# Optimization experiments

Measured on AMD Instinct MI355X. Metric: run time of the kernel, lower is better.

Reference implementation:

```python
import jax, jax.numpy as jnp
import numpy as np

THRESH = 0.3
OUT_THRESH = 0.3
LENS = 0.5  # surrogate-gradient window (ActFun in snn-delays repo)


@jax.custom_vjp
def spike(x):
    # Heaviside spike with rectangular surrogate gradient
    return (x > 0.0).astype(x.dtype)

def _spike_fwd(x):
    return spike(x), x

def _spike_bwd(x, g):
    return (g * (jnp.abs(x) < LENS).astype(g.dtype),)

spike.defvjp(_spike_fwd, _spike_bwd)


def setup_inputs() -> dict:
    key = jax.random.key(0)
    ks = jax.random.split(key, 7)
    B, T, I, H, O = 256, 50, 1024, 2048, 20
    # binary input spikes (rate ~0.2), as an SNN would receive
    inp = (jax.random.uniform(ks[0], (B, T, I)) < 0.2).astype(jnp.float32)
    # Linear(in, out, bias=False) -> weight [out, in], Kaiming-uniform-ish init
    w_ih = jax.random.uniform(ks[1], (H, I), minval=-1.0, maxval=1.0) / np.sqrt(I)
    w_hh = jax.random.uniform(ks[2], (H, H), minval=-1.0, maxval=1.0) / np.sqrt(H)
    w_ho = jax.random.uniform(ks[3], (O, H), minval=-1.0, maxval=1.0) / np.sqrt(H)
    tau_m_h = 0.83 + 0.1 * jax.random.normal(ks[4], (H,))
    tau_m_o = 0.83 + 0.1 * jax.random.normal(ks[5], (O,))
    return {"input": inp, "w_ih": w_ih, "w_hh": w_hh, "w_ho": w_ho,
            "tau_m_h": tau_m_h, "tau_m_o": tau_m_o}


def _rsnn_forward(inp, w_ih, w_hh, w_ho, tau_m_h, tau_m_o):
    B, T, I = inp.shape
    H = w_ih.shape[0]
    O = w_ho.shape[0]
    alpha_h = jnp.exp(-1.0 / tau_m_h)  # [H]
    alpha_o = jnp.exp(-1.0 / tau_m_o)  # [O]
    zH = jnp.zeros((B, H), inp.dtype)
    zO = jnp.zeros((B, O), inp.dtype)

    def step(carry, x_t):
        h_mem, h_spk, o_mem, o_spk, o_sum, mot = carry
        # hidden membrane update: input + recurrent + decayed (reset-gated) mem
        h_mem = (x_t @ w_ih.T) + (h_spk @ w_hh.T) + h_mem * alpha_h * (1.0 - h_spk)
        h_spk = spike(h_mem - THRESH)
        # output membrane update
        o_mem = o_mem * alpha_o * (1.0 - o_spk) + h_spk @ w_ho.T
        o_spk = spike(o_mem - OUT_THRESH)
        o_sum = o_sum + o_spk
        mot = mot + jax.nn.softmax(o_mem, axis=1)
        return (h_mem, h_spk, o_mem, o_spk, o_sum, mot), None

    init = (zH, zH, zO, zO, zO, zO)
    (h_mem, h_spk, o_mem, o_spk, o_sum, mot), _ = jax.lax.scan(
        step, init, jnp.swapaxes(inp, 0, 1))  # scan over time [T,B,I]
    return o_sum / T, mot


def reference(input, w_ih, w_hh, w_ho, tau_m_h, tau_m_o):
    return _rsnn_forward(input, w_ih, w_hh, w_ho, tau_m_h, tau_m_o)
```

## Files before the change

kernel.cpp:

```cpp
#include <hip/hip_runtime.h>
#include <stdint.h>
#include <math.h>


#define B_   256
#define T_   50
#define I_   1024
#define H_   2048
#define O_   20
#define XIN_T  262144
#define XS_BUF 524288
#define WNT 589824
#define WPL 196608

typedef __attribute__((ext_vector_type(4))) int intx4;
typedef long long ll_t;

__device__ __forceinline__ int digit_of(float v, int p) {
  int W = (int)rintf(v * 134217728.0f);
  int c0 = ((W + 128) & 255) - 128;
  int W1 = (W - c0) >> 8;
  int c1 = ((W1 + 128) & 255) - 128;
  int W2 = (W1 - c1) >> 8;
  return (p == 0) ? c0 : (p == 1) ? c1 : W2;
}

__global__ void prep_w(const float* __restrict__ w_ih,
                       const float* __restrict__ w_hh,
                       int8_t* __restrict__ Wtl) {
  int blk = blockIdx.x;
  int n = blk / 9, kg = blk % 9;
  int k9 = (kg * 256 + (int)threadIdx.x) * 4;
  int p = k9 / 3072, kk = k9 % 3072;
  const float* src = (kk < 1024) ? (w_ih + n * I_ + kk)
                                 : (w_hh + n * H_ + (kk - 1024));
  float4 v = *(const float4*)src;
  int d0 = digit_of(v.x, p) & 255;
  int d1 = digit_of(v.y, p) & 255;
  int d2 = digit_of(v.z, p) & 255;
  int d3 = digit_of(v.w, p) & 255;
  int packed = d0 | (d1 << 8) | (d2 << 16) | (d3 << 24);
  size_t off = (size_t)(n >> 6) * WNT + (size_t)p * WPL + (kk >> 6) * 4096 +
               (n & 63) * 64 + (kk & 63);
  *(int*)(Wtl + off) = packed;
}

__global__ void init_k(int8_t* __restrict__ Xin, int8_t* __restrict__ Xs,
                       float* __restrict__ Hm, const float* __restrict__ input,
                       const float* __restrict__ tau_h,
                       const float* __restrict__ tau_o,
                       float* __restrict__ AlphaH, float* __restrict__ AlphaO,
                       const float* __restrict__ w_ho, double* __restrict__ WhoD,
                       float* __restrict__ Om, float* __restrict__ Osp,
                       float* __restrict__ Osu, float* __restrict__ Mo) {
  int id = blockIdx.x * 256 + threadIdx.x;
  {
    int b = id >> 8, i4 = (id & 255) * 4;
    for (int t = 0; t < T_; ++t) {
      float4 v = *(const float4*)(input + ((size_t)(b * T_ + t) << 10) + i4);
      uchar4 pk;
      pk.x = v.x > 0.5f ? 1 : 0;
      pk.y = v.y > 0.5f ? 1 : 0;
      pk.z = v.z > 0.5f ? 1 : 0;
      pk.w = v.w > 0.5f ? 1 : 0;
      *(uchar4*)(Xin + (size_t)t * XIN_T + (b >> 6) * 65536 + (i4 >> 6) * 4096 +
                 (b & 63) * 64 + (i4 & 63)) = pk;
    }
  }
  *(double*)(Xs + (size_t)id * 8) = 0.0;
  *(float4*)(Hm + (size_t)id * 8) = make_float4(0.f, 0.f, 0.f, 0.f);
  *(float4*)(Hm + (size_t)id * 8 + 4) = make_float4(0.f, 0.f, 0.f, 0.f);
  if (id < 32 * O_ * 64) {
    int nt = id / 1280, rem = id % 1280, o = rem / 64, hl = rem & 63;
    WhoD[id] = (double)w_ho[o * H_ + nt * 64 + hl];
  }
  if (id < H_) AlphaH[id] = (float)exp((double)(-1.0f / tau_h[id]));
  if (id < O_) AlphaO[id] = (float)exp((double)(-1.0f / tau_o[id]));
  if (id < B_ * O_) {
    Om[id] = 0.f; Osp[id] = 0.f; Osu[id] = 0.f; Mo[id] = 0.f;
  }
}

__global__ __launch_bounds__(512, 1) void step_k(
    const int8_t* __restrict__ Wtl, const int8_t* __restrict__ Xin,
    int8_t* __restrict__ Xs, float* __restrict__ Hm, double* __restrict__ Po,
    const double* __restrict__ WhoD, const float* __restrict__ AlphaH,
    const float* __restrict__ AlphaO, float* __restrict__ Om,
    float* __restrict__ Osp, float* __restrict__ Osu, float* __restrict__ Mo,
    int t) {
  __shared__ double WhoL[1280];
  __shared__ __align__(16) int8_t red[49152];
  __shared__ int8_t spk_lT[2048];
  __shared__ float om_l[O_];

  const int j = blockIdx.x;
  const int nt = (j & 7) * 4 + (j >> 6);
  const int mt = (j >> 3) & 7;
  const int tid = threadIdx.x;
  const int l = tid & 63, wv = tid >> 6;
  const int c = wv >> 2, k = wv & 3;
  const int r_ = l & 15, q = l >> 4;

  for (int i = tid; i < 1280; i += 512) WhoL[i] = WhoD[nt * 1280 + i];

  if (t > 0 && tid < O_) {
    const double* pp = Po + ((size_t)(((t - 1) & 1) * 256 + j) * 32) * 20 + tid;
    double s = 0.0;
#pragma unroll
    for (int n2 = 0; n2 < 32; ++n2) s += pp[n2 * 20];
    float r = (float)s;
    float m = Om[j * O_ + tid] * AlphaO[tid] * (1.0f - Osp[j * O_ + tid]) + r;
    om_l[tid] = m;
  }
  __syncthreads();
  if (t > 0 && tid < O_) {
    float m = om_l[tid];
    float mx = om_l[0];
#pragma unroll
    for (int o = 1; o < O_; ++o) mx = fmaxf(mx, om_l[o]);
    float se = 0.f;
#pragma unroll
    for (int o = 0; o < O_; ++o) se += expf(om_l[o] - mx);
    float sp = (m - 0.3f) > 0.f ? 1.f : 0.f;
    Om[j * O_ + tid] = m;
    Osp[j * O_ + tid] = sp;
    Osu[j * O_ + tid] += sp;
    Mo[j * O_ + tid] += expf(m - mx) / se;
  }

  const int arow = ((mt & 1) * 32 + r_) * 64 + q * 16;
  const int8_t* Ain = Xin + (size_t)t * XIN_T + (mt >> 1) * 65536 + arow;
  const int8_t* Asp = Xs + (size_t)(t & 1) * XS_BUF + (mt >> 1) * 131072 + arow;
  const int8_t* Bw = Wtl + (size_t)nt * WNT + (c * 32 + r_) * 64 + q * 16;
  const int u0 = k * 12;

  intx4 acc[2][2][3];
#pragma unroll
  for (int fr = 0; fr < 2; ++fr)
#pragma unroll
    for (int fc = 0; fc < 2; ++fc)
#pragma unroll
      for (int p = 0; p < 3; ++p) acc[fr][fc][p] = (intx4){0, 0, 0, 0};

  intx4 a[2][2], b[2][2][3];
  {
    const int8_t* ap = (u0 < 16) ? (Ain + u0 * 4096) : (Asp + (u0 - 16) * 4096);
    a[0][0] = *(const intx4*)ap;
    a[0][1] = *(const intx4*)(ap + 1024);
    const int8_t* bp = Bw + u0 * 4096;
#pragma unroll
    for (int p = 0; p < 3; ++p)
#pragma unroll
      for (int fc = 0; fc < 2; ++fc)
        b[0][fc][p] = *(const intx4*)(bp + p * WPL + fc * 1024);
  }
#pragma unroll
  for (int i = 0; i < 12; ++i) {
    const int cur = i & 1, nxt = cur ^ 1;
    if (i < 11) {
      const int un = u0 + i + 1;
      const int8_t* ap = (un < 16) ? (Ain + un * 4096) : (Asp + (un - 16) * 4096);
      a[nxt][0] = *(const intx4*)ap;
      a[nxt][1] = *(const intx4*)(ap + 1024);
      const int8_t* bp = Bw + un * 4096;
#pragma unroll
      for (int p = 0; p < 3; ++p)
#pragma unroll
        for (int fc = 0; fc < 2; ++fc)
          b[nxt][fc][p] = *(const intx4*)(bp + p * WPL + fc * 1024);
    }
#pragma unroll
    for (int p = 0; p < 3; ++p)
#pragma unroll
      for (int fc = 0; fc < 2; ++fc) {
        acc[0][fc][p] = __builtin_amdgcn_mfma_i32_16x16x64_i8(
            a[cur][0], b[cur][fc][p], acc[0][fc][p], 0, 0, 0);
        acc[1][fc][p] = __builtin_amdgcn_mfma_i32_16x16x64_i8(
            a[cur][1], b[cur][fc][p], acc[1][fc][p], 0, 0, 0);
      }
  }

#define REDP(s, idx) (red + (((c * 2 + (s)) * 12 + (idx)) * 64 + l) * 16)
  if (k == 1 || k == 3) {
    const int s = k >> 1;
#pragma unroll
    for (int fr = 0; fr < 2; ++fr)
#pragma unroll
      for (int fc = 0; fc < 2; ++fc)
#pragma unroll
        for (int p = 0; p < 3; ++p)
          *(intx4*)REDP(s, fr * 6 + fc * 3 + p) = acc[fr][fc][p];
  }
  __syncthreads();
  if (k == 0 || k == 2) {
    const int s = k >> 1;
#pragma unroll
    for (int fr = 0; fr < 2; ++fr)
#pragma unroll
      for (int fc = 0; fc < 2; ++fc)
#pragma unroll
        for (int p = 0; p < 3; ++p)
          acc[fr][fc][p] = acc[fr][fc][p] +
                           *(const intx4*)REDP(s, fr * 6 + fc * 3 + p);
    if (k == 2) {
#pragma unroll
      for (int fr = 0; fr < 2; ++fr)
#pragma unroll
        for (int fc = 0; fc < 2; ++fc)
#pragma unroll
          for (int p = 0; p < 3; ++p)
            *(intx4*)REDP(1, fr * 6 + fc * 3 + p) = acc[fr][fc][p];
    }
  }
  __syncthreads();

  if (k == 0) {
    int8_t* Xw = Xs + (size_t)((t + 1) & 1) * XS_BUF;
    const int h0 = nt * 64 + c * 32 + r_;
#pragma unroll
    for (int fc = 0; fc < 2; ++fc) {
      const int h = h0 + fc * 16;
      const float alpha = AlphaH[h];
#pragma unroll
      for (int fr = 0; fr < 2; ++fr) {
        intx4 s0 = acc[fr][fc][0] + *(const intx4*)REDP(1, fr * 6 + fc * 3 + 0);
        intx4 s1 = acc[fr][fc][1] + *(const intx4*)REDP(1, fr * 6 + fc * 3 + 1);
        intx4 s2 = acc[fr][fc][2] + *(const intx4*)REDP(1, fr * 6 + fc * 3 + 2);
        unsigned spkpack = 0;
#pragma unroll
        for (int jj = 0; jj < 4; ++jj) {
          ll_t Sv = (ll_t)s0[jj] + ((ll_t)s1[jj] << 8) + ((ll_t)s2[jj] << 16);
          float M = (float)((double)Sv * 7.450580596923828125e-9);
          const int brow = mt * 32 + fr * 16 + q * 4 + jj;
          const int idx = brow * H_ + h;
          float hp = Hm[idx];
          float spf = (hp - 0.3f) > 0.f ? 1.f : 0.f;
          float hm = M + hp * alpha * (1.0f - spf);
          Hm[idx] = hm;
          unsigned spk = (hm - 0.3f) > 0.f ? 1u : 0u;
          Xw[(brow >> 6) * 131072 + (h >> 6) * 4096 + (brow & 63) * 64 +
             (h & 63)] = (int8_t)spk;
          spkpack |= spk << (8 * jj);
        }
        *(unsigned*)(spk_lT + (c * 32 + fc * 16 + r_) * 32 + fr * 16 + q * 4) =
            spkpack;
      }
    }
  }
  __syncthreads();

  if (tid < 128) {
    const int bl = tid >> 2, og = (tid & 3) * 5;
    const double* W0 = WhoL + og * 64;
    double a0 = 0, a1 = 0, a2 = 0, a3 = 0, a4 = 0;
#pragma unroll
    for (int hl = 0; hl < 64; ++hl) {
      double m = (double)spk_lT[hl * 32 + bl];
      a0 += m * W0[hl];
      a1 += m * W0[64 + hl];
      a2 += m * W0[128 + hl];
      a3 += m * W0[192 + hl];
      a4 += m * W0[256 + hl];
    }
    double* dst =
        Po + ((size_t)((t & 1) * 256 + mt * 32 + bl) * 32 + nt) * 20 + og;
    dst[0] = a0; dst[1] = a1; dst[2] = a2; dst[3] = a3; dst[4] = a4;
  }
#undef REDP
}

__global__ void final_k(const double* __restrict__ Po,
                        const float* __restrict__ AlphaO,
                        const float* __restrict__ Om,
                        const float* __restrict__ Osp,
                        const float* __restrict__ Osu,
                        const float* __restrict__ Mo, float* __restrict__ out) {
  __shared__ float om_l[O_];
  const int j = blockIdx.x, tid = threadIdx.x;
  if (tid < O_) {
    const double* pp = Po + ((size_t)(256 + j) * 32) * 20 + tid;
    double s = 0.0;
#pragma unroll
    for (int n2 = 0; n2 < 32; ++n2) s += pp[n2 * 20];
    float r = (float)s;
    float m = Om[j * O_ + tid] * AlphaO[tid] * (1.0f - Osp[j * O_ + tid]) + r;
    om_l[tid] = m;
  }
  __syncthreads();
  if (tid < O_) {
    float m = om_l[tid];
    float mx = om_l[0];
#pragma unroll
    for (int o = 1; o < O_; ++o) mx = fmaxf(mx, om_l[o]);
    float se = 0.f;
#pragma unroll
    for (int o = 0; o < O_; ++o) se += expf(om_l[o] - mx);
    float sp = (m - 0.3f) > 0.f ? 1.f : 0.f;
    out[j * O_ + tid] = (Osu[j * O_ + tid] + sp) / 50.0f;
    out[B_ * O_ + j * O_ + tid] = Mo[j * O_ + tid] + expf(m - mx) / se;
  }
}

extern "C" void kernel_launch(void* const* d_in, const int* in_sizes, int n_in,
                              void* d_out, int out_size, void* d_ws, size_t ws_size,
                              hipStream_t stream) {
  const float* input = (const float*)d_in[0];
  const float* w_ih  = (const float*)d_in[1];
  const float* w_hh  = (const float*)d_in[2];
  const float* w_ho  = (const float*)d_in[3];
  const float* tau_h = (const float*)d_in[4];
  const float* tau_o = (const float*)d_in[5];

  char* ws = (char*)d_ws;
  int8_t* Wtl    = (int8_t*)(ws);
  int8_t* Xin    = (int8_t*)(ws + 18874368);
  int8_t* Xs     = (int8_t*)(ws + 31981568);
  double* Po     = (double*)(ws + 33030144);
  float*  Hm     = (float*)(ws + 35651584);
  double* WhoD   = (double*)(ws + 37748736);
  float*  AlphaH = (float*)(ws + 38076416);
  float*  AlphaO = (float*)(ws + 38084608);
  float*  Om     = (float*)(ws + 38084736);
  float*  Osp    = (float*)(ws + 38105216);
  float*  Osu    = (float*)(ws + 38125696);
  float*  Mo     = (float*)(ws + 38146176);
  float*  out    = (float*)d_out;

  prep_w<<<2048 * 9, 256, 0, stream>>>(w_ih, w_hh, Wtl);
  init_k<<<256, 256, 0, stream>>>(Xin, Xs, Hm, input, tau_h, tau_o, AlphaH,
                                  AlphaO, w_ho, WhoD, Om, Osp, Osu, Mo);
  for (int t = 0; t < T_; ++t) {
    step_k<<<256, 512, 0, stream>>>(Wtl, Xin, Xs, Hm, Po, WhoD, AlphaH, AlphaO,
                                    Om, Osp, Osu, Mo, t);
  }
  final_k<<<256, 64, 0, stream>>>(Po, AlphaO, Om, Osp, Osu, Mo, out);
}
```

Measured before the change: 1.110 ms.

## Halve hidden-neuron tile per block and split K across eight waves

Hidden columns per block drop from 64 to 32, so the grid doubles from 256 to 512 blocks. Each block now splits the K dimension across all 8 waves, each handling 6 chunks, and combines them with a three-level tree reduction in shared memory. The weight layout, w_ho staging and output partial-sum buffers are re-tiled for 32-wide tiles, and launch bounds are relaxed so more blocks can share a CU. This aims to fill more CUs and shorten each block's serial MFMA chain, at the cost of more reduction barriers and twice as many output partials to sum.

```diff
diff --git a/kernel.cpp b/kernel.cpp
--- a/kernel.cpp
+++ b/kernel.cpp
@@ -10,8 +10,8 @@
 #define O_   20
 #define XIN_T  262144
 #define XS_BUF 524288
-#define WNT 589824
-#define WPL 196608
+#define WNT 294912
+#define WPL 98304
 
 typedef __attribute__((ext_vector_type(4))) int intx4;
 typedef long long ll_t;
@@ -40,8 +40,8 @@
   int d2 = digit_of(v.z, p) & 255;
   int d3 = digit_of(v.w, p) & 255;
   int packed = d0 | (d1 << 8) | (d2 << 16) | (d3 << 24);
-  size_t off = (size_t)(n >> 6) * WNT + (size_t)p * WPL + (kk >> 6) * 4096 +
-               (n & 63) * 64 + (kk & 63);
+  size_t off = (size_t)(n >> 5) * WNT + (size_t)p * WPL + (kk >> 6) * 2048 +
+               (n & 31) * 64 + (kk & 63);
   *(int*)(Wtl + off) = packed;
 }
 
@@ -70,9 +70,9 @@
   *(double*)(Xs + (size_t)id * 8) = 0.0;
   *(float4*)(Hm + (size_t)id * 8) = make_float4(0.f, 0.f, 0.f, 0.f);
   *(float4*)(Hm + (size_t)id * 8 + 4) = make_float4(0.f, 0.f, 0.f, 0.f);
-  if (id < 32 * O_ * 64) {
-    int nt = id / 1280, rem = id % 1280, o = rem / 64, hl = rem & 63;
-    WhoD[id] = (double)w_ho[o * H_ + nt * 64 + hl];
+  if (id < 64 * O_ * 32) {
+    int nt = id / 640, rem = id % 640, o = rem / 32, hl = rem & 31;
+    WhoD[id] = (double)w_ho[o * H_ + nt * 32 + hl];
   }
   if (id < H_) AlphaH[id] = (float)exp((double)(-1.0f / tau_h[id]));
   if (id < O_) AlphaO[id] = (float)exp((double)(-1.0f / tau_o[id]));
@@ -81,39 +81,38 @@
   }
 }
 
-__global__ __launch_bounds__(512, 1) void step_k(
+__global__ __launch_bounds__(512, 4) void step_k(
     const int8_t* __restrict__ Wtl, const int8_t* __restrict__ Xin,
     int8_t* __restrict__ Xs, float* __restrict__ Hm, double* __restrict__ Po,
     const double* __restrict__ WhoD, const float* __restrict__ AlphaH,
     const float* __restrict__ AlphaO, float* __restrict__ Om,
     float* __restrict__ Osp, float* __restrict__ Osu, float* __restrict__ Mo,
     int t) {
-  __shared__ double WhoL[1280];
+  __shared__ double WhoL[640];
   __shared__ __align__(16) int8_t red[49152];
-  __shared__ int8_t spk_lT[2048];
+  __shared__ int8_t spk_lT[1024];
   __shared__ float om_l[O_];
 
   const int j = blockIdx.x;
-  const int nt = (j & 7) * 4 + (j >> 6);
-  const int mt = (j >> 3) & 7;
+  const int nt = (j & 7) * 8 + ((j >> 3) & 7);
+  const int mt = j >> 6;
   const int tid = threadIdx.x;
-  const int l = tid & 63, wv = tid >> 6;
-  const int c = wv >> 2, k = wv & 3;
+  const int l = tid & 63, k = tid >> 6;
   const int r_ = l & 15, q = l >> 4;
 
-  for (int i = tid; i < 1280; i += 512) WhoL[i] = WhoD[nt * 1280 + i];
-
-  if (t > 0 && tid < O_) {
-    const double* pp = Po + ((size_t)(((t - 1) & 1) * 256 + j) * 32) * 20 + tid;
+  for (int i = tid; i < 640; i += 512) WhoL[i] = WhoD[nt * 640 + i];
+
+  if (t > 0 && j < B_ && tid < O_) {
+    const double* pp = Po + ((size_t)(((t - 1) & 1) * 256 + j) * 64) * 20 + tid;
     double s = 0.0;
 #pragma unroll
-    for (int n2 = 0; n2 < 32; ++n2) s += pp[n2 * 20];
+    for (int n2 = 0; n2 < 64; ++n2) s += pp[n2 * 20];
     float r = (float)s;
     float m = Om[j * O_ + tid] * AlphaO[tid] * (1.0f - Osp[j * O_ + tid]) + r;
     om_l[tid] = m;
   }
   __syncthreads();
-  if (t > 0 && tid < O_) {
+  if (t > 0 && j < B_ && tid < O_) {
     float m = om_l[tid];
     float mx = om_l[0];
 #pragma unroll
@@ -131,8 +130,8 @@
   const int arow = ((mt & 1) * 32 + r_) * 64 + q * 16;
   const int8_t* Ain = Xin + (size_t)t * XIN_T + (mt >> 1) * 65536 + arow;
   const int8_t* Asp = Xs + (size_t)(t & 1) * XS_BUF + (mt >> 1) * 131072 + arow;
-  const int8_t* Bw = Wtl + (size_t)nt * WNT + (c * 32 + r_) * 64 + q * 16;
-  const int u0 = k * 12;
+  const int8_t* Bw = Wtl + (size_t)nt * WNT + r_ * 64 + q * 16;
+  const int u0 = k * 6;
 
   intx4 acc[2][2][3];
 #pragma unroll
@@ -147,7 +146,7 @@
     const int8_t* ap = (u0 < 16) ? (Ain + u0 * 4096) : (Asp + (u0 - 16) * 4096);
     a[0][0] = *(const intx4*)ap;
     a[0][1] = *(const intx4*)(ap + 1024);
-    const int8_t* bp = Bw + u0 * 4096;
+    const int8_t* bp = Bw + u0 * 2048;
 #pragma unroll
     for (int p = 0; p < 3; ++p)
 #pragma unroll
@@ -155,14 +154,14 @@
         b[0][fc][p] = *(const intx4*)(bp + p * WPL + fc * 1024);
   }
 #pragma unroll
-  for (int i = 0; i < 12; ++i) {
+  for (int i = 0; i < 6; ++i) {
     const int cur = i & 1, nxt = cur ^ 1;
-    if (i < 11) {
+    if (i < 5) {
       const int un = u0 + i + 1;
       const int8_t* ap = (un < 16) ? (Ain + un * 4096) : (Asp + (un - 16) * 4096);
       a[nxt][0] = *(const intx4*)ap;
       a[nxt][1] = *(const intx4*)(ap + 1024);
-      const int8_t* bp = Bw + un * 4096;
+      const int8_t* bp = Bw + un * 2048;
 #pragma unroll
       for (int p = 0; p < 3; ++p)
 #pragma unroll
@@ -180,52 +179,72 @@
       }
   }
 
-#define REDP(s, idx) (red + (((c * 2 + (s)) * 12 + (idx)) * 64 + l) * 16)
-  if (k == 1 || k == 3) {
-    const int s = k >> 1;
-#pragma unroll
-    for (int fr = 0; fr < 2; ++fr)
-#pragma unroll
-      for (int fc = 0; fc < 2; ++fc)
-#pragma unroll
-        for (int p = 0; p < 3; ++p)
-          *(intx4*)REDP(s, fr * 6 + fc * 3 + p) = acc[fr][fc][p];
-  }
-  __syncthreads();
-  if (k == 0 || k == 2) {
-    const int s = k >> 1;
-#pragma unroll
-    for (int fr = 0; fr < 2; ++fr)
-#pragma unroll
-      for (int fc = 0; fc < 2; ++fc)
-#pragma unroll
-        for (int p = 0; p < 3; ++p)
-          acc[fr][fc][p] = acc[fr][fc][p] +
-                           *(const intx4*)REDP(s, fr * 6 + fc * 3 + p);
-    if (k == 2) {
-#pragma unroll
-      for (int fr = 0; fr < 2; ++fr)
-#pragma unroll
-        for (int fc = 0; fc < 2; ++fc)
-#pragma unroll
-          for (int p = 0; p < 3; ++p)
-            *(intx4*)REDP(1, fr * 6 + fc * 3 + p) = acc[fr][fc][p];
-    }
+#define REDP(slot, idx) (red + (((slot) * 12 + (idx)) * 64 + l) * 16)
+#define ACCIDX(fr, fc, p) ((fr) * 6 + (fc) * 3 + (p))
+  if (k & 1) {
+#pragma unroll
+    for (int fr = 0; fr < 2; ++fr)
+#pragma unroll
+      for (int fc = 0; fc < 2; ++fc)
+#pragma unroll
+        for (int p = 0; p < 3; ++p)
+          *(intx4*)REDP(k >> 1, ACCIDX(fr, fc, p)) = acc[fr][fc][p];
+  }
+  __syncthreads();
+  if (!(k & 1)) {
+#pragma unroll
+    for (int fr = 0; fr < 2; ++fr)
+#pragma unroll
+      for (int fc = 0; fc < 2; ++fc)
+#pragma unroll
+        for (int p = 0; p < 3; ++p)
+          acc[fr][fc][p] =
+              acc[fr][fc][p] + *(const intx4*)REDP(k >> 1, ACCIDX(fr, fc, p));
+  }
+  __syncthreads();
+  if (k == 2 || k == 6) {
+#pragma unroll
+    for (int fr = 0; fr < 2; ++fr)
+#pragma unroll
+      for (int fc = 0; fc < 2; ++fc)
+#pragma unroll
+        for (int p = 0; p < 3; ++p)
+          *(intx4*)REDP(k >> 2, ACCIDX(fr, fc, p)) = acc[fr][fc][p];
+  }
+  __syncthreads();
+  if (k == 0 || k == 4) {
+#pragma unroll
+    for (int fr = 0; fr < 2; ++fr)
+#pragma unroll
+      for (int fc = 0; fc < 2; ++fc)
+#pragma unroll
+        for (int p = 0; p < 3; ++p)
+          acc[fr][fc][p] =
+              acc[fr][fc][p] + *(const intx4*)REDP(k >> 2, ACCIDX(fr, fc, p));
+  }
+  __syncthreads();
+  if (k == 4) {
+#pragma unroll
+    for (int fr = 0; fr < 2; ++fr)
+#pragma unroll
+      for (int fc = 0; fc < 2; ++fc)
+#pragma unroll
+        for (int p = 0; p < 3; ++p)
+          *(intx4*)REDP(0, ACCIDX(fr, fc, p)) = acc[fr][fc][p];
   }
   __syncthreads();
 
   if (k == 0) {
     int8_t* Xw = Xs + (size_t)((t + 1) & 1) * XS_BUF;
-    const int h0 = nt * 64 + c * 32 + r_;
 #pragma unroll
     for (int fc = 0; fc < 2; ++fc) {
-      const int h = h0 + fc * 16;
+      const int h = nt * 32 + fc * 16 + r_;
       const float alpha = AlphaH[h];
 #pragma unroll
       for (int fr = 0; fr < 2; ++fr) {
-        intx4 s0 = acc[fr][fc][0] + *(const intx4*)REDP(1, fr * 6 + fc * 3 + 0);
-        intx4 s1 = acc[fr][fc][1] + *(const intx4*)REDP(1, fr * 6 + fc * 3 + 1);
-        intx4 s2 = acc[fr][fc][2] + *(const intx4*)REDP(1, fr * 6 + fc * 3 + 2);
+        intx4 s0 = acc[fr][fc][0] + *(const intx4*)REDP(0, ACCIDX(fr, fc, 0));
+        intx4 s1 = acc[fr][fc][1] + *(const intx4*)REDP(0, ACCIDX(fr, fc, 1));
+        intx4 s2 = acc[fr][fc][2] + *(const intx4*)REDP(0, ACCIDX(fr, fc, 2));
         unsigned spkpack = 0;
 #pragma unroll
         for (int jj = 0; jj < 4; ++jj) {
@@ -242,8 +261,7 @@
              (h & 63)] = (int8_t)spk;
           spkpack |= spk << (8 * jj);
         }
-        *(unsigned*)(spk_lT + (c * 32 + fc * 16 + r_) * 32 + fr * 16 + q * 4) =
-            spkpack;
+        *(unsigned*)(spk_lT + (fc * 16 + r_) * 32 + fr * 16 + q * 4) = spkpack;
       }
     }
   }
@@ -251,22 +269,23 @@
 
   if (tid < 128) {
     const int bl = tid >> 2, og = (tid & 3) * 5;
-    const double* W0 = WhoL + og * 64;
+    const double* W0 = WhoL + og * 32;
     double a0 = 0, a1 = 0, a2 = 0, a3 = 0, a4 = 0;
 #pragma unroll
-    for (int hl = 0; hl < 64; ++hl) {
+    for (int hl = 0; hl < 32; ++hl) {
       double m = (double)spk_lT[hl * 32 + bl];
       a0 += m * W0[hl];
-      a1 += m * W0[64 + hl];
-      a2 += m * W0[128 + hl];
-      a3 += m * W0[192 + hl];
-      a4 += m * W0[256 + hl];
+      a1 += m * W0[32 + hl];
+      a2 += m * W0[64 + hl];
+      a3 += m * W0[96 + hl];
+      a4 += m * W0[128 + hl];
     }
     double* dst =
-        Po + ((size_t)((t & 1) * 256 + mt * 32 + bl) * 32 + nt) * 20 + og;
+        Po + ((size_t)((t & 1) * 256 + mt * 32 + bl) * 64 + nt) * 20 + og;
     dst[0] = a0; dst[1] = a1; dst[2] = a2; dst[3] = a3; dst[4] = a4;
   }
 #undef REDP
+#undef ACCIDX
 }
 
 __global__ void final_k(const double* __restrict__ Po,
@@ -278,10 +297,10 @@
   __shared__ float om_l[O_];
   const int j = blockIdx.x, tid = threadIdx.x;
   if (tid < O_) {
-    const double* pp = Po + ((size_t)(256 + j) * 32) * 20 + tid;
+    const double* pp = Po + ((size_t)(256 + j) * 64) * 20 + tid;
     double s = 0.0;
 #pragma unroll
-    for (int n2 = 0; n2 < 32; ++n2) s += pp[n2 * 20];
+    for (int n2 = 0; n2 < 64; ++n2) s += pp[n2 * 20];
     float r = (float)s;
     float m = Om[j * O_ + tid] * AlphaO[tid] * (1.0f - Osp[j * O_ + tid]) + r;
     om_l[tid] = m;
@@ -316,21 +335,21 @@
   int8_t* Xin    = (int8_t*)(ws + 18874368);
   int8_t* Xs     = (int8_t*)(ws + 31981568);
   double* Po     = (double*)(ws + 33030144);
-  float*  Hm     = (float*)(ws + 35651584);
-  double* WhoD   = (double*)(ws + 37748736);
-  float*  AlphaH = (float*)(ws + 38076416);
-  float*  AlphaO = (float*)(ws + 38084608);
-  float*  Om     = (float*)(ws + 38084736);
-  float*  Osp    = (float*)(ws + 38105216);
-  float*  Osu    = (float*)(ws + 38125696);
-  float*  Mo     = (float*)(ws + 38146176);
+  float*  Hm     = (float*)(ws + 38273024);
+  double* WhoD   = (double*)(ws + 40370176);
+  float*  AlphaH = (float*)(ws + 40697856);
+  float*  AlphaO = (float*)(ws + 40706048);
+  float*  Om     = (float*)(ws + 40706176);
+  float*  Osp    = (float*)(ws + 40726656);
+  float*  Osu    = (float*)(ws + 40747136);
+  float*  Mo     = (float*)(ws + 40767616);
   float*  out    = (float*)d_out;
 
   prep_w<<<2048 * 9, 256, 0, stream>>>(w_ih, w_hh, Wtl);
   init_k<<<256, 256, 0, stream>>>(Xin, Xs, Hm, input, tau_h, tau_o, AlphaH,
                                   AlphaO, w_ho, WhoD, Om, Osp, Osu, Mo);
   for (int t = 0; t < T_; ++t) {
-    step_k<<<256, 512, 0, stream>>>(Wtl, Xin, Xs, Hm, Po, WhoD, AlphaH, AlphaO,
+    step_k<<<512, 512, 0, stream>>>(Wtl, Xin, Xs, Hm, Po, WhoD, AlphaH, AlphaO,
                                     Om, Osp, Osu, Mo, t);
   }
   final_k<<<256, 64, 0, stream>>>(Po, AlphaO, Om, Osp, Osu, Mo, out);
```

Measured after the change: 1.108 ms. Within noise of the previous version (-0.2%).

## Fuse timestep loop into persistent kernel with per-XCD atomic barriers

Applied to the files above, without the earlier changes.

Replaces the 50 per-timestep launches and the final kernel with one persistent kernel. Each block reads its XCC_ID register and takes a slot via an atomic counter, so each XCD owns a 32-row batch group and synchronises only within itself through spin-wait counters. Membrane state, decay factors and output-neuron state stay in registers instead of round-tripping through global memory. This removes launch overhead and global state traffic, but depends on all 256 blocks being co-resident and on an exactly even block-to-XCD distribution; any imbalance or lack of co-residency would deadlock or corrupt results.

```diff
diff --git a/kernel.cpp b/kernel.cpp
--- a/kernel.cpp
+++ b/kernel.cpp
@@ -9,7 +9,6 @@
 #define H_   2048
 #define O_   20
 #define XIN_T  262144
-#define XS_BUF 524288
 #define WNT 589824
 #define WPL 196608
 
@@ -46,13 +45,9 @@
 }
 
 __global__ void init_k(int8_t* __restrict__ Xin, int8_t* __restrict__ Xs,
-                       float* __restrict__ Hm, const float* __restrict__ input,
-                       const float* __restrict__ tau_h,
-                       const float* __restrict__ tau_o,
-                       float* __restrict__ AlphaH, float* __restrict__ AlphaO,
+                       const float* __restrict__ input,
                        const float* __restrict__ w_ho, double* __restrict__ WhoD,
-                       float* __restrict__ Om, float* __restrict__ Osp,
-                       float* __restrict__ Osu, float* __restrict__ Mo) {
+                       unsigned* __restrict__ Ctl) {
   int id = blockIdx.x * 256 + threadIdx.x;
   {
     int b = id >> 8, i4 = (id & 255) * 4;
@@ -67,237 +62,297 @@
                  (b & 63) * 64 + (i4 & 63)) = pk;
     }
   }
-  *(double*)(Xs + (size_t)id * 8) = 0.0;
-  *(float4*)(Hm + (size_t)id * 8) = make_float4(0.f, 0.f, 0.f, 0.f);
-  *(float4*)(Hm + (size_t)id * 8 + 4) = make_float4(0.f, 0.f, 0.f, 0.f);
+  *(float4*)(Xs + (size_t)id * 16) = make_float4(0.f, 0.f, 0.f, 0.f);
   if (id < 32 * O_ * 64) {
     int nt = id / 1280, rem = id % 1280, o = rem / 64, hl = rem & 63;
     WhoD[id] = (double)w_ho[o * H_ + nt * 64 + hl];
   }
-  if (id < H_) AlphaH[id] = (float)exp((double)(-1.0f / tau_h[id]));
-  if (id < O_) AlphaO[id] = (float)exp((double)(-1.0f / tau_o[id]));
-  if (id < B_ * O_) {
-    Om[id] = 0.f; Osp[id] = 0.f; Osu[id] = 0.f; Mo[id] = 0.f;
-  }
-}
-
-__global__ __launch_bounds__(512, 1) void step_k(
+  if (id < 24) Ctl[id] = 0u;
+}
+
+__global__ __launch_bounds__(512, 2) void rsnn_pers(
     const int8_t* __restrict__ Wtl, const int8_t* __restrict__ Xin,
-    int8_t* __restrict__ Xs, float* __restrict__ Hm, double* __restrict__ Po,
-    const double* __restrict__ WhoD, const float* __restrict__ AlphaH,
-    const float* __restrict__ AlphaO, float* __restrict__ Om,
-    float* __restrict__ Osp, float* __restrict__ Osu, float* __restrict__ Mo,
-    int t) {
+    int8_t* __restrict__ Xs, double* __restrict__ Po,
+    const double* __restrict__ WhoD, const float* __restrict__ tau_h,
+    const float* __restrict__ tau_o, unsigned* __restrict__ Ctl,
+    float* __restrict__ out) {
   __shared__ double WhoL[1280];
   __shared__ __align__(16) int8_t red[49152];
   __shared__ int8_t spk_lT[2048];
   __shared__ float om_l[O_];
-
-  const int j = blockIdx.x;
-  const int nt = (j & 7) * 4 + (j >> 6);
-  const int mt = (j >> 3) & 7;
+  __shared__ unsigned binfo[2];
+
   const int tid = threadIdx.x;
+  if (tid == 0) {
+    unsigned xcc;
+    asm volatile("s_getreg_b32 %0, hwreg(HW_REG_XCC_ID)" : "=s"(xcc));
+    xcc &= 7u;
+    unsigned slot = __hip_atomic_fetch_add(&Ctl[xcc], 1u, __ATOMIC_RELAXED,
+                                           __HIP_MEMORY_SCOPE_AGENT);
+    binfo[0] = xcc;
+    binfo[1] = slot & 31u;
+  }
+  __syncthreads();
+  const int xcd = (int)binfo[0], slot = (int)binfo[1];
+
   const int l = tid & 63, wv = tid >> 6;
   const int c = wv >> 2, k = wv & 3;
   const int r_ = l & 15, q = l >> 4;
-
-  for (int i = tid; i < 1280; i += 512) WhoL[i] = WhoD[nt * 1280 + i];
-
-  if (t > 0 && tid < O_) {
-    const double* pp = Po + ((size_t)(((t - 1) & 1) * 256 + j) * 32) * 20 + tid;
-    double s = 0.0;
-#pragma unroll
-    for (int n2 = 0; n2 < 32; ++n2) s += pp[n2 * 20];
-    float r = (float)s;
-    float m = Om[j * O_ + tid] * AlphaO[tid] * (1.0f - Osp[j * O_ + tid]) + r;
-    om_l[tid] = m;
+  const int bg = xcd;
+
+  for (int i = tid; i < 1280; i += 512) WhoL[i] = WhoD[slot * 1280 + i];
+
+  float alphaO_r = 0.f;
+  if (tid < O_) {
+    float rr = -1.0f / tau_o[tid];
+    alphaO_r = (float)exp((double)rr);
+  }
+  float Om_r = 0.f, Osu_r = 0.f, Mo_r = 0.f;
+  float alpha_f[2];
+#pragma unroll
+  for (int fc = 0; fc < 2; ++fc) {
+    int h = slot * 64 + c * 32 + fc * 16 + r_;
+    float rr = -1.0f / tau_h[h];
+    alpha_f[fc] = (float)exp((double)rr);
+  }
+  float hm_r[2][2][4];
+#pragma unroll
+  for (int fc = 0; fc < 2; ++fc)
+#pragma unroll
+    for (int fr = 0; fr < 2; ++fr)
+#pragma unroll
+      for (int jj = 0; jj < 4; ++jj) hm_r[fc][fr][jj] = 0.f;
+
+  const int arow_in = ((bg & 1) * 32 + r_) * 64 + q * 16;
+  const int arow_sp = r_ * 64 + q * 16;
+  const int8_t* AinB = Xin + (bg >> 1) * 65536 + arow_in;
+  int8_t* XsX = Xs + xcd * 131072;
+  const int8_t* Bw = Wtl + (size_t)slot * WNT + (c * 32 + r_) * 64 + q * 16;
+  const int u0 = k * 12;
+  const int brow = xcd * 32 + slot;
+
+  for (int t = 0; t < T_; ++t) {
+    if (t > 0) {
+      if (tid == 0) {
+        unsigned v;
+        do {
+          __builtin_amdgcn_s_sleep(2);
+          v = __hip_atomic_load(&Ctl[16 + xcd], __ATOMIC_RELAXED,
+                                __HIP_MEMORY_SCOPE_AGENT);
+        } while (v < (unsigned)t);
+      }
+      __syncthreads();
+      const int par = (t - 1) & 1;
+      if (tid < O_) {
+        const double* pp =
+            Po + ((((size_t)xcd * 2 + par) * 32) * 32 + slot) * 20 + tid;
+        double s = 0.0;
+#pragma unroll
+        for (int s2 = 0; s2 < 32; ++s2) s += pp[(size_t)s2 * 640];
+        float r = (float)s;
+        float spo = (Om_r - 0.3f) > 0.f ? 1.f : 0.f;
+        float m = Om_r * alphaO_r * (1.0f - spo) + r;
+        om_l[tid] = m;
+      }
+      __syncthreads();
+      if (tid < O_) {
+        float m = om_l[tid];
+        float mx = om_l[0];
+#pragma unroll
+        for (int o = 1; o < O_; ++o) mx = fmaxf(mx, om_l[o]);
+        float se = 0.f;
+#pragma unroll
+        for (int o = 0; o < O_; ++o) se += expf(om_l[o] - mx);
+        float sp = (m - 0.3f) > 0.f ? 1.f : 0.f;
+        Om_r = m;
+        Osu_r += sp;
+        Mo_r += expf(m - mx) / se;
+      }
+      __syncthreads();
+    }
+
+    const int8_t* Ain = AinB + (size_t)t * XIN_T;
+    const int8_t* Asp = XsX + (t & 1) * 65536 + arow_sp;
+
+    intx4 acc[2][2][3];
+#pragma unroll
+    for (int fr = 0; fr < 2; ++fr)
+#pragma unroll
+      for (int fc = 0; fc < 2; ++fc)
+#pragma unroll
+        for (int p = 0; p < 3; ++p) acc[fr][fc][p] = (intx4){0, 0, 0, 0};
+
+    intx4 a[2][2], b[2][2][3];
+    {
+      const int8_t* ap = (u0 < 16) ? (Ain + u0 * 4096) : (Asp + (u0 - 16) * 2048);
+      a[0][0] = *(const intx4*)ap;
+      a[0][1] = *(const intx4*)(ap + 1024);
+      const int8_t* bp = Bw + u0 * 4096;
+#pragma unroll
+      for (int p = 0; p < 3; ++p)
+#pragma unroll
+        for (int fc = 0; fc < 2; ++fc)
+          b[0][fc][p] = *(const intx4*)(bp + p * WPL + fc * 1024);
+    }
+#pragma unroll
+    for (int i = 0; i < 12; ++i) {
+      const int cur = i & 1, nxt = cur ^ 1;
+      if (i < 11) {
+        const int un = u0 + i + 1;
+        const int8_t* ap =
+            (un < 16) ? (Ain + un * 4096) : (Asp + (un - 16) * 2048);
+        a[nxt][0] = *(const intx4*)ap;
+        a[nxt][1] = *(const intx4*)(ap + 1024);
+        const int8_t* bp = Bw + un * 4096;
+#pragma unroll
+        for (int p = 0; p < 3; ++p)
+#pragma unroll
+          for (int fc = 0; fc < 2; ++fc)
+            b[nxt][fc][p] = *(const intx4*)(bp + p * WPL + fc * 1024);
+      }
+#pragma unroll
+      for (int p = 0; p < 3; ++p)
+#pragma unroll
+        for (int fc = 0; fc < 2; ++fc) {
+          acc[0][fc][p] = __builtin_amdgcn_mfma_i32_16x16x64_i8(
+              a[cur][0], b[cur][fc][p], acc[0][fc][p], 0, 0, 0);
+          acc[1][fc][p] = __builtin_amdgcn_mfma_i32_16x16x64_i8(
+              a[cur][1], b[cur][fc][p], acc[1][fc][p], 0, 0, 0);
+        }
+    }
+
+#define REDP(s, idx) (red + (((c * 2 + (s)) * 12 + (idx)) * 64 + l) * 16)
+#define ACCIDX(fr, fc, p) ((fr) * 6 + (fc) * 3 + (p))
+    if (k == 1 || k == 3) {
+      const int s = k >> 1;
+#pragma unroll
+      for (int fr = 0; fr < 2; ++fr)
+#pragma unroll
+        for (int fc = 0; fc < 2; ++fc)
+#pragma unroll
+          for (int p = 0; p < 3; ++p)
+            *(intx4*)REDP(s, ACCIDX(fr, fc, p)) = acc[fr][fc][p];
+    }
+    __syncthreads();
+    if (k == 0 || k == 2) {
+      const int s = k >> 1;
+#pragma unroll
+      for (int fr = 0; fr < 2; ++fr)
+#pragma unroll
+        for (int fc = 0; fc < 2; ++fc)
+#pragma unroll
+          for (int p = 0; p < 3; ++p)
+            acc[fr][fc][p] =
+                acc[fr][fc][p] + *(const intx4*)REDP(s, ACCIDX(fr, fc, p));
+      if (k == 2) {
+#pragma unroll
+        for (int fr = 0; fr < 2; ++fr)
+#pragma unroll
+          for (int fc = 0; fc < 2; ++fc)
+#pragma unroll
+            for (int p = 0; p < 3; ++p)
+              *(intx4*)REDP(1, ACCIDX(fr, fc, p)) = acc[fr][fc][p];
+      }
+    }
+    __syncthreads();
+
+    if (k == 0) {
+      int8_t* Xw = XsX + ((t + 1) & 1) * 65536 + slot * 2048;
+#pragma unroll
+      for (int fc = 0; fc < 2; ++fc) {
+        const int hcol = c * 32 + fc * 16 + r_;
+#pragma unroll
+        for (int fr = 0; fr < 2; ++fr) {
+          intx4 s0 = acc[fr][fc][0] + *(const intx4*)REDP(1, ACCIDX(fr, fc, 0));
+          intx4 s1 = acc[fr][fc][1] + *(const intx4*)REDP(1, ACCIDX(fr, fc, 1));
+          intx4 s2 = acc[fr][fc][2] + *(const intx4*)REDP(1, ACCIDX(fr, fc, 2));
+          unsigned spkpack = 0;
+#pragma unroll
+          for (int jj = 0; jj < 4; ++jj) {
+            ll_t Sv = (ll_t)s0[jj] + ((ll_t)s1[jj] << 8) + ((ll_t)s2[jj] << 16);
+            float M = (float)((double)Sv * 7.450580596923828125e-9);
+            float hp = hm_r[fc][fr][jj];
+            float spf = (hp - 0.3f) > 0.f ? 1.f : 0.f;
+            float hm = M + hp * alpha_f[fc] * (1.0f - spf);
+            hm_r[fc][fr][jj] = hm;
+            unsigned spk = (hm - 0.3f) > 0.f ? 1u : 0u;
+            int row = fr * 16 + q * 4 + jj;
+            Xw[row * 64 + hcol] = (int8_t)spk;
+            spkpack |= spk << (8 * jj);
+          }
+          *(unsigned*)(spk_lT + (c * 32 + fc * 16 + r_) * 32 + fr * 16 + q * 4) =
+              spkpack;
+        }
+      }
+    }
+    __syncthreads();
+
+    if (tid < 128) {
+      const int bl = tid >> 2, og = (tid & 3) * 5;
+      const double* W0 = WhoL + og * 64;
+      double a0 = 0, a1 = 0, a2 = 0, a3 = 0, a4 = 0;
+#pragma unroll
+      for (int hl = 0; hl < 64; ++hl) {
+        double m = (double)spk_lT[hl * 32 + bl];
+        a0 += m * W0[hl];
+        a1 += m * W0[64 + hl];
+        a2 += m * W0[128 + hl];
+        a3 += m * W0[192 + hl];
+        a4 += m * W0[256 + hl];
+      }
+      double* dst =
+          Po + ((((size_t)xcd * 2 + (t & 1)) * 32 + slot) * 32 + bl) * 20 + og;
+      dst[0] = a0; dst[1] = a1; dst[2] = a2; dst[3] = a3; dst[4] = a4;
+    }
+#undef REDP
+#undef ACCIDX
+
+    __builtin_amdgcn_s_waitcnt(0);
+    __syncthreads();
+    if (tid == 0) {
+      unsigned old = __hip_atomic_fetch_add(&Ctl[8 + xcd], 1u, __ATOMIC_RELAXED,
+                                            __HIP_MEMORY_SCOPE_AGENT);
+      if (old == (unsigned)(32 * (t + 1) - 1))
+        __hip_atomic_store(&Ctl[16 + xcd], (unsigned)(t + 1), __ATOMIC_RELAXED,
+                           __HIP_MEMORY_SCOPE_AGENT);
+    }
+  }
+
+  if (tid == 0) {
+    unsigned v;
+    do {
+      __builtin_amdgcn_s_sleep(2);
+      v = __hip_atomic_load(&Ctl[16 + xcd], __ATOMIC_RELAXED,
+                            __HIP_MEMORY_SCOPE_AGENT);
+    } while (v < (unsigned)T_);
   }
   __syncthreads();
-  if (t > 0 && tid < O_) {
-    float m = om_l[tid];
-    float mx = om_l[0];
-#pragma unroll
-    for (int o = 1; o < O_; ++o) mx = fmaxf(mx, om_l[o]);
-    float se = 0.f;
-#pragma unroll
-    for (int o = 0; o < O_; ++o) se += expf(om_l[o] - mx);
-    float sp = (m - 0.3f) > 0.f ? 1.f : 0.f;
-    Om[j * O_ + tid] = m;
-    Osp[j * O_ + tid] = sp;
-    Osu[j * O_ + tid] += sp;
-    Mo[j * O_ + tid] += expf(m - mx) / se;
-  }
-
-  const int arow = ((mt & 1) * 32 + r_) * 64 + q * 16;
-  const int8_t* Ain = Xin + (size_t)t * XIN_T + (mt >> 1) * 65536 + arow;
-  const int8_t* Asp = Xs + (size_t)(t & 1) * XS_BUF + (mt >> 1) * 131072 + arow;
-  const int8_t* Bw = Wtl + (size_t)nt * WNT + (c * 32 + r_) * 64 + q * 16;
-  const int u0 = k * 12;
-
-  intx4 acc[2][2][3];
-#pragma unroll
-  for (int fr = 0; fr < 2; ++fr)
-#pragma unroll
-    for (int fc = 0; fc < 2; ++fc)
-#pragma unroll
-      for (int p = 0; p < 3; ++p) acc[fr][fc][p] = (intx4){0, 0, 0, 0};
-
-  intx4 a[2][2], b[2][2][3];
   {
-    const int8_t* ap = (u0 < 16) ? (Ain + u0 * 4096) : (Asp + (u0 - 16) * 4096);
-    a[0][0] = *(const intx4*)ap;
-    a[0][1] = *(const intx4*)(ap + 1024);
-    const int8_t* bp = Bw + u0 * 4096;
-#pragma unroll
-    for (int p = 0; p < 3; ++p)
-#pragma unroll
-      for (int fc = 0; fc < 2; ++fc)
-        b[0][fc][p] = *(const intx4*)(bp + p * WPL + fc * 1024);
-  }
-#pragma unroll
-  for (int i = 0; i < 12; ++i) {
-    const int cur = i & 1, nxt = cur ^ 1;
-    if (i < 11) {
-      const int un = u0 + i + 1;
-      const int8_t* ap = (un < 16) ? (Ain + un * 4096) : (Asp + (un - 16) * 4096);
-      a[nxt][0] = *(const intx4*)ap;
-      a[nxt][1] = *(const intx4*)(ap + 1024);
-      const int8_t* bp = Bw + un * 4096;
-#pragma unroll
-      for (int p = 0; p < 3; ++p)
-#pragma unroll
-        for (int fc = 0; fc < 2; ++fc)
-          b[nxt][fc][p] = *(const intx4*)(bp + p * WPL + fc * 1024);
-    }
-#pragma unroll
-    for (int p = 0; p < 3; ++p)
-#pragma unroll
-      for (int fc = 0; fc < 2; ++fc) {
-        acc[0][fc][p] = __builtin_amdgcn_mfma_i32_16x16x64_i8(
-            a[cur][0], b[cur][fc][p], acc[0][fc][p], 0, 0, 0);
-        acc[1][fc][p] = __builtin_amdgcn_mfma_i32_16x16x64_i8(
-            a[cur][1], b[cur][fc][p], acc[1][fc][p], 0, 0, 0);
-      }
-  }
-
-#define REDP(s, idx) (red + (((c * 2 + (s)) * 12 + (idx)) * 64 + l) * 16)
-  if (k == 1 || k == 3) {
-    const int s = k >> 1;
-#pragma unroll
-    for (int fr = 0; fr < 2; ++fr)
-#pragma unroll
-      for (int fc = 0; fc < 2; ++fc)
-#pragma unroll
-        for (int p = 0; p < 3; ++p)
-          *(intx4*)REDP(s, fr * 6 + fc * 3 + p) = acc[fr][fc][p];
-  }
-  __syncthreads();
-  if (k == 0 || k == 2) {
-    const int s = k >> 1;
-#pragma unroll
-    for (int fr = 0; fr < 2; ++fr)
-#pragma unroll
-      for (int fc = 0; fc < 2; ++fc)
-#pragma unroll
-        for (int p = 0; p < 3; ++p)
-          acc[fr][fc][p] = acc[fr][fc][p] +
-                           *(const intx4*)REDP(s, fr * 6 + fc * 3 + p);
-    if (k == 2) {
-#pragma unroll
-      for (int fr = 0; fr < 2; ++fr)
-#pragma unroll
-        for (int fc = 0; fc < 2; ++fc)
-#pragma unroll
-          for (int p = 0; p < 3; ++p)
-            *(intx4*)REDP(1, fr * 6 + fc * 3 + p) = acc[fr][fc][p];
-    }
-  }
-  __syncthreads();
-
-  if (k == 0) {
-    int8_t* Xw = Xs + (size_t)((t + 1) & 1) * XS_BUF;
-    const int h0 = nt * 64 + c * 32 + r_;
-#pragma unroll
-    for (int fc = 0; fc < 2; ++fc) {
-      const int h = h0 + fc * 16;
-      const float alpha = AlphaH[h];
-#pragma unroll
-      for (int fr = 0; fr < 2; ++fr) {
-        intx4 s0 = acc[fr][fc][0] + *(const intx4*)REDP(1, fr * 6 + fc * 3 + 0);
-        intx4 s1 = acc[fr][fc][1] + *(const intx4*)REDP(1, fr * 6 + fc * 3 + 1);
-        intx4 s2 = acc[fr][fc][2] + *(const intx4*)REDP(1, fr * 6 + fc * 3 + 2);
-        unsigned spkpack = 0;
-#pragma unroll
-        for (int jj = 0; jj < 4; ++jj) {
-          ll_t Sv = (ll_t)s0[jj] + ((ll_t)s1[jj] << 8) + ((ll_t)s2[jj] << 16);
-          float M = (float)((double)Sv * 7.450580596923828125e-9);
-          const int brow = mt * 32 + fr * 16 + q * 4 + jj;
-          const int idx = brow * H_ + h;
-          float hp = Hm[idx];
-          float spf = (hp - 0.3f) > 0.f ? 1.f : 0.f;
-          float hm = M + hp * alpha * (1.0f - spf);
-          Hm[idx] = hm;
-          unsigned spk = (hm - 0.3f) > 0.f ? 1u : 0u;
-          Xw[(brow >> 6) * 131072 + (h >> 6) * 4096 + (brow & 63) * 64 +
-             (h & 63)] = (int8_t)spk;
-          spkpack |= spk << (8 * jj);
-        }
-        *(unsigned*)(spk_lT + (c * 32 + fc * 16 + r_) * 32 + fr * 16 + q * 4) =
-            spkpack;
-      }
-    }
-  }
-  __syncthreads();
-
-  if (tid < 128) {
-    const int bl = tid >> 2, og = (tid & 3) * 5;
-    const double* W0 = WhoL + og * 64;
-    double a0 = 0, a1 = 0, a2 = 0, a3 = 0, a4 = 0;
-#pragma unroll
-    for (int hl = 0; hl < 64; ++hl) {
-      double m = (double)spk_lT[hl * 32 + bl];
-      a0 += m * W0[hl];
-      a1 += m * W0[64 + hl];
-      a2 += m * W0[128 + hl];
-      a3 += m * W0[192 + hl];
-      a4 += m * W0[256 + hl];
-    }
-    double* dst =
-        Po + ((size_t)((t & 1) * 256 + mt * 32 + bl) * 32 + nt) * 20 + og;
-    dst[0] = a0; dst[1] = a1; dst[2] = a2; dst[3] = a3; dst[4] = a4;
-  }
-#undef REDP
-}
-
-__global__ void final_k(const double* __restrict__ Po,
-                        const float* __restrict__ AlphaO,
-                        const float* __restrict__ Om,
-                        const float* __restrict__ Osp,
-                        const float* __restrict__ Osu,
-                        const float* __restrict__ Mo, float* __restrict__ out) {
-  __shared__ float om_l[O_];
-  const int j = blockIdx.x, tid = threadIdx.x;
-  if (tid < O_) {
-    const double* pp = Po + ((size_t)(256 + j) * 32) * 20 + tid;
-    double s = 0.0;
-#pragma unroll
-    for (int n2 = 0; n2 < 32; ++n2) s += pp[n2 * 20];
-    float r = (float)s;
-    float m = Om[j * O_ + tid] * AlphaO[tid] * (1.0f - Osp[j * O_ + tid]) + r;
-    om_l[tid] = m;
-  }
-  __syncthreads();
-  if (tid < O_) {
-    float m = om_l[tid];
-    float mx = om_l[0];
-#pragma unroll
-    for (int o = 1; o < O_; ++o) mx = fmaxf(mx, om_l[o]);
-    float se = 0.f;
-#pragma unroll
-    for (int o = 0; o < O_; ++o) se += expf(om_l[o] - mx);
-    float sp = (m - 0.3f) > 0.f ? 1.f : 0.f;
-    out[j * O_ + tid] = (Osu[j * O_ + tid] + sp) / 50.0f;
-    out[B_ * O_ + j * O_ + tid] = Mo[j * O_ + tid] + expf(m - mx) / se;
+    const int par = (T_ - 1) & 1;
+    if (tid < O_) {
+      const double* pp =
+          Po + ((((size_t)xcd * 2 + par) * 32) * 32 + slot) * 20 + tid;
+      double s = 0.0;
+#pragma unroll
+      for (int s2 = 0; s2 < 32; ++s2) s += pp[(size_t)s2 * 640];
+      float r = (float)s;
+      float spo = (Om_r - 0.3f) > 0.f ? 1.f : 0.f;
+      float m = Om_r * alphaO_r * (1.0f - spo) + r;
+      om_l[tid] = m;
+    }
+    __syncthreads();
+    if (tid < O_) {
+      float m = om_l[tid];
+      float mx = om_l[0];
+#pragma unroll
+      for (int o = 1; o < O_; ++o) mx = fmaxf(mx, om_l[o]);
+      float se = 0.f;
+#pragma unroll
+      for (int o = 0; o < O_; ++o) se += expf(om_l[o] - mx);
+      float sp = (m - 0.3f) > 0.f ? 1.f : 0.f;
+      out[brow * O_ + tid] = (Osu_r + sp) / 50.0f;
+      out[B_ * O_ + brow * O_ + tid] = Mo_r + expf(m - mx) / se;
+    }
   }
 }
 
@@ -312,26 +367,16 @@
   const float* tau_o = (const float*)d_in[5];
 
   char* ws = (char*)d_ws;
-  int8_t* Wtl    = (int8_t*)(ws);
-  int8_t* Xin    = (int8_t*)(ws + 18874368);
-  int8_t* Xs     = (int8_t*)(ws + 31981568);
-  double* Po     = (double*)(ws + 33030144);
-  float*  Hm     = (float*)(ws + 35651584);
-  double* WhoD   = (double*)(ws + 37748736);
-  float*  AlphaH = (float*)(ws + 38076416);
-  float*  AlphaO = (float*)(ws + 38084608);
-  float*  Om     = (float*)(ws + 38084736);
-  float*  Osp    = (float*)(ws + 38105216);
-  float*  Osu    = (float*)(ws + 38125696);
-  float*  Mo     = (float*)(ws + 38146176);
-  float*  out    = (float*)d_out;
+  int8_t*   Wtl  = (int8_t*)(ws);
+  int8_t*   Xin  = (int8_t*)(ws + 18874368);
+  int8_t*   Xs   = (int8_t*)(ws + 31981568);
+  double*   Po   = (double*)(ws + 33030144);
+  double*   WhoD = (double*)(ws + 39583744);
+  unsigned* Ctl  = (unsigned*)(ws + 39911424);
+  float*    out  = (float*)d_out;
 
   prep_w<<<2048 * 9, 256, 0, stream>>>(w_ih, w_hh, Wtl);
-  init_k<<<256, 256, 0, stream>>>(Xin, Xs, Hm, input, tau_h, tau_o, AlphaH,
-                                  AlphaO, w_ho, WhoD, Om, Osp, Osu, Mo);
-  for (int t = 0; t < T_; ++t) {
-    step_k<<<256, 512, 0, stream>>>(Wtl, Xin, Xs, Hm, Po, WhoD, AlphaH, AlphaO,
-                                    Om, Osp, Osu, Mo, t);
-  }
-  final_k<<<256, 64, 0, stream>>>(Po, AlphaO, Om, Osp, Osu, Mo, out);
-}
+  init_k<<<256, 256, 0, stream>>>(Xin, Xs, input, w_ho, WhoD, Ctl);
+  rsnn_pers<<<256, 512, 0, stream>>>(Wtl, Xin, Xs, Po, WhoD, tau_h, tau_o,
+                                     Ctl, out);
+}
```

New measurement: 1.989 ms. 79.2% more time.
